# Optimization experiments

Hardware: AMD Instinct MI355X
Metric: run time of the kernel (lower is better)

Reference implementation:

```python
import jax, jax.numpy as jnp
import numpy as np

N_NODES = 100000
N_EDGES = 1600000
IN_DIM = 128
OUT_DIM = 128


def setup_inputs() -> dict:
    key = jax.random.key(0)
    k1, k2, k3, k4, k5 = jax.random.split(key, 5)
    h = jax.random.normal(k1, (N_NODES, IN_DIM), dtype=jnp.float32)
    # nn.Linear(in_dim, out_dim): W [out, in], b [out]
    W = jax.random.normal(k2, (OUT_DIM, IN_DIM), dtype=jnp.float32) * (1.0 / np.sqrt(IN_DIM))
    b = jax.random.normal(k3, (OUT_DIM,), dtype=jnp.float32) * 0.01
    edge_src = jax.random.randint(k4, (N_EDGES,), 0, N_NODES, dtype=jnp.int32)
    edge_dst = jax.random.randint(k5, (N_EDGES,), 0, N_NODES, dtype=jnp.int32)
    return {"h": h, "W": W, "b": b, "edge_src": edge_src, "edge_dst": edge_dst}


def reference(h, W, b, edge_src, edge_dst):
    n = h.shape[0]
    # in-degree of each node (edges point src -> dst), clamped to >= 1
    deg = jax.ops.segment_sum(jnp.ones_like(edge_dst, dtype=h.dtype), edge_dst, num_segments=n)
    norm = jnp.power(jnp.clip(deg, 1.0), -0.5)[:, None]  # [N, 1]
    hn = h * norm
    # copy_u + sum: gather source features, scatter-add to destinations (SpMM)
    agg = jax.ops.segment_sum(hn[edge_src], edge_dst, num_segments=n)  # [N, in_dim]
    out = (agg * norm) @ W.T + b
    return out
```

## Files before the change

kernel.cpp:

```cpp
#include <hip/hip_runtime.h>
#include <hip/hip_fp16.h>

#define DIM 128
#define TSH 8
#define TSZ 256
#define EBLK 4096

typedef _Float16 half8_t __attribute__((ext_vector_type(8)));
typedef float f32x4 __attribute__((ext_vector_type(4)));


__global__ __launch_bounds__(256) void hist_a(const int* __restrict__ dst,
                                              int* __restrict__ gh,
                                              int ne, int nblk, int nt) {
    __shared__ int h[512];
    int t = threadIdx.x;
    h[t] = 0; h[t + 256] = 0;
    __syncthreads();
    int i0 = blockIdx.x * EBLK + t;
#pragma unroll
    for (int u = 0; u < 16; ++u) {
        int i = i0 + u * 256;
        if (i < ne) atomicAdd(&h[dst[i] >> TSH], 1);
    }
    __syncthreads();
    for (int k = t; k < nt; k += 256) gh[k * nblk + blockIdx.x] = h[k];
}

__global__ __launch_bounds__(256) void scan_a(int* __restrict__ g,
                                              int* __restrict__ bsum, int M) {
    __shared__ int wsum[4];
    int t = threadIdx.x;
    int base = blockIdx.x * 1024 + t * 4;
    int4 v;
    if (base + 3 < M) v = *(const int4*)(g + base);
    else {
        v.x = (base + 0 < M) ? g[base + 0] : 0;
        v.y = (base + 1 < M) ? g[base + 1] : 0;
        v.z = (base + 2 < M) ? g[base + 2] : 0;
        v.w = (base + 3 < M) ? g[base + 3] : 0;
    }
    int s3 = v.x + v.y + v.z + v.w;
    int lane = t & 63, wv = t >> 6;
    int x = s3;
#pragma unroll
    for (int off = 1; off < 64; off <<= 1) {
        int y = __shfl_up(x, off, 64);
        if (lane >= off) x += y;
    }
    if (lane == 63) wsum[wv] = x;
    __syncthreads();
    int woff = 0;
    for (int i = 0; i < wv; ++i) woff += wsum[i];
    int ex = woff + x - s3;
    int4 o;
    o.x = ex; o.y = ex + v.x; o.z = o.y + v.y; o.w = o.z + v.z;
    if (base + 3 < M) *(int4*)(g + base) = o;
    else {
        if (base + 0 < M) g[base + 0] = o.x;
        if (base + 1 < M) g[base + 1] = o.y;
        if (base + 2 < M) g[base + 2] = o.z;
        if (base + 3 < M) g[base + 3] = o.w;
    }
    if (t == 0) bsum[blockIdx.x] = wsum[0] + wsum[1] + wsum[2] + wsum[3];
}

__global__ __launch_bounds__(256) void scanb_wprep(int* __restrict__ bsum, int nb,
                                                   const float* __restrict__ W,
                                                   _Float16* __restrict__ Wf) {
    if (blockIdx.x == 0) {
        __shared__ int s[256];
        int t = threadIdx.x;
        int d = (t < nb) ? bsum[t] : 0;
        s[t] = d;
        __syncthreads();
        for (int off = 1; off < 256; off <<= 1) {
            int v = (t >= off) ? s[t - off] : 0;
            __syncthreads();
            s[t] += v;
            __syncthreads();
        }
        if (t < nb) bsum[t] = s[t] - d;
    } else {
        int idx = (blockIdx.x - 1) * 256 + threadIdx.x;
        int tile = idx >> 8;
        int kk = (idx >> 6) & 3;
        int lane = idx & 63;
        int nn = lane & 15, quad = lane >> 4;
        const float* wr = W + (tile * 16 + nn) * DIM + kk * 32 + quad * 8;
        _Float16* o = Wf + (size_t)idx * 8;
#pragma unroll
        for (int j = 0; j < 8; ++j) o[j] = (_Float16)wr[j];
    }
}

__global__ __launch_bounds__(256) void scatter_b(const int* __restrict__ src,
                                                 const int* __restrict__ dst,
                                                 const int* __restrict__ gh,
                                                 const int* __restrict__ gb,
                                                 unsigned* __restrict__ tbuf,
                                                 int ne, int nblk) {
    __shared__ int h[512];
    int t = threadIdx.x;
    h[t] = 0; h[t + 256] = 0;
    __syncthreads();
    int i0 = blockIdx.x * EBLK + t;
#pragma unroll
    for (int u = 0; u < 16; ++u) {
        int i = i0 + u * 256;
        if (i < ne) {
            int d = dst[i];
            int key = d >> TSH;
            int r = atomicAdd(&h[key], 1);
            int idx = key * nblk + blockIdx.x;
            int pos = gh[idx] + gb[idx >> 10] + r;
            tbuf[pos] = ((unsigned)src[i] << TSH) | (unsigned)(d & (TSZ - 1));
        }
    }
}

__global__ __launch_bounds__(256) void tile_sort(const unsigned* __restrict__ tbuf,
                                                 const int* __restrict__ gh,
                                                 const int* __restrict__ gb,
                                                 int* __restrict__ ebuf,
                                                 int* __restrict__ row_start,
                                                 int n, int ne, int nblk, int nt) {
    __shared__ int hist[TSZ];
    __shared__ int cur[TSZ];
    __shared__ int ps[TSZ];
    int t = threadIdx.x;
    int tile = blockIdx.x;
    int i0 = tile * nblk;
    int ts = gh[i0] + gb[i0 >> 10];
    int i1 = (tile + 1) * nblk;
    int te = (tile + 1 < nt) ? gh[i1] + gb[i1 >> 10] : ne;
    hist[t] = 0;
    __syncthreads();
    for (int i = ts + t; i < te; i += 256)
        atomicAdd(&hist[tbuf[i] & (TSZ - 1)], 1);
    __syncthreads();
    int d = hist[t];
    ps[t] = d;
    __syncthreads();
    for (int off = 1; off < 256; off <<= 1) {
        int v = (t >= off) ? ps[t - off] : 0;
        __syncthreads();
        ps[t] += v;
        __syncthreads();
    }
    int ex = ps[t] - d;
    cur[t] = ex;
    int node = tile * TSZ + t;
    if (node <= n) row_start[node] = ts + ex;
    __syncthreads();
    for (int i = ts + t; i < te; i += 256) {
        unsigned p = tbuf[i];
        int dl = (int)(p & (TSZ - 1));
        int r = atomicAdd(&cur[dl], 1);
        ebuf[ts + r] = (int)(p >> TSH);
    }
}

__global__ __launch_bounds__(256) void hn_pack(const float* __restrict__ h,
                                               const int* __restrict__ rs,
                                               float2* __restrict__ hn, int n32) {
    int i = blockIdx.x * 256 + threadIdx.x;
    if (i >= n32) return;
    int node = i >> 5;
    int d = rs[node + 1] - rs[node];
    float sc = rsqrtf((float)(d > 1 ? d : 1));
    float4 v = ((const float4*)h)[i];
    union { __half2 h2[2]; float2 f2; } u;
    u.h2[0] = __floats2half2_rn(v.x * sc, v.y * sc);
    u.h2[1] = __floats2half2_rn(v.z * sc, v.w * sc);
    hn[i] = u.f2;
}

__global__ __launch_bounds__(512) void gather_gemm(const float2* __restrict__ hn,
                                                   const int* __restrict__ ebuf,
                                                   const int* __restrict__ rs,
                                                   const _Float16* __restrict__ Wf,
                                                   const float* __restrict__ b,
                                                   float* __restrict__ out, int n) {
    __shared__ _Float16 xs[64 * 136];
    int tid = threadIdx.x;
    int g = tid >> 5, lane = tid & 31;

#pragma unroll
    for (int it = 0; it < 4; ++it) {
        int row = it * 16 + g;
        int node = blockIdx.x * 64 + row;
        union { __half2 h2[2]; float2 f2; } u;
        if (node < n) {
            int s0 = rs[node];
            int s1 = rs[node + 1];
            __half2 a0 = __floats2half2_rn(0.f, 0.f), a1 = a0;
            int i = s0;
            for (; i + 7 < s1; i += 8) {
                int e0 = ebuf[i], e1 = ebuf[i + 1], e2 = ebuf[i + 2], e3 = ebuf[i + 3];
                int e4 = ebuf[i + 4], e5 = ebuf[i + 5], e6 = ebuf[i + 6], e7 = ebuf[i + 7];
                float2 r0 = hn[(size_t)e0 * 32 + lane];
                float2 r1 = hn[(size_t)e1 * 32 + lane];
                float2 r2 = hn[(size_t)e2 * 32 + lane];
                float2 r3 = hn[(size_t)e3 * 32 + lane];
                float2 r4 = hn[(size_t)e4 * 32 + lane];
                float2 r5 = hn[(size_t)e5 * 32 + lane];
                float2 r6 = hn[(size_t)e6 * 32 + lane];
                float2 r7 = hn[(size_t)e7 * 32 + lane];
                const __half2* q0 = (const __half2*)&r0;
                const __half2* q1 = (const __half2*)&r1;
                const __half2* q2 = (const __half2*)&r2;
                const __half2* q3 = (const __half2*)&r3;
                const __half2* q4 = (const __half2*)&r4;
                const __half2* q5 = (const __half2*)&r5;
                const __half2* q6 = (const __half2*)&r6;
                const __half2* q7 = (const __half2*)&r7;
                a0 = __hadd2(a0, q0[0]); a1 = __hadd2(a1, q0[1]);
                a0 = __hadd2(a0, q1[0]); a1 = __hadd2(a1, q1[1]);
                a0 = __hadd2(a0, q2[0]); a1 = __hadd2(a1, q2[1]);
                a0 = __hadd2(a0, q3[0]); a1 = __hadd2(a1, q3[1]);
                a0 = __hadd2(a0, q4[0]); a1 = __hadd2(a1, q4[1]);
                a0 = __hadd2(a0, q5[0]); a1 = __hadd2(a1, q5[1]);
                a0 = __hadd2(a0, q6[0]); a1 = __hadd2(a1, q6[1]);
                a0 = __hadd2(a0, q7[0]); a1 = __hadd2(a1, q7[1]);
            }
            for (; i + 3 < s1; i += 4) {
                int e0 = ebuf[i], e1 = ebuf[i + 1], e2 = ebuf[i + 2], e3 = ebuf[i + 3];
                float2 r0 = hn[(size_t)e0 * 32 + lane];
                float2 r1 = hn[(size_t)e1 * 32 + lane];
                float2 r2 = hn[(size_t)e2 * 32 + lane];
                float2 r3 = hn[(size_t)e3 * 32 + lane];
                const __half2* q0 = (const __half2*)&r0;
                const __half2* q1 = (const __half2*)&r1;
                const __half2* q2 = (const __half2*)&r2;
                const __half2* q3 = (const __half2*)&r3;
                a0 = __hadd2(a0, q0[0]); a1 = __hadd2(a1, q0[1]);
                a0 = __hadd2(a0, q1[0]); a1 = __hadd2(a1, q1[1]);
                a0 = __hadd2(a0, q2[0]); a1 = __hadd2(a1, q2[1]);
                a0 = __hadd2(a0, q3[0]); a1 = __hadd2(a1, q3[1]);
            }
            for (; i < s1; ++i) {
                int e0 = ebuf[i];
                float2 r0 = hn[(size_t)e0 * 32 + lane];
                const __half2* q0 = (const __half2*)&r0;
                a0 = __hadd2(a0, q0[0]); a1 = __hadd2(a1, q0[1]);
            }
            int dn = s1 - s0;
            float nd = rsqrtf((float)(dn > 1 ? dn : 1));
            float2 f0 = __half22float2(a0), f1 = __half22float2(a1);
            u.h2[0] = __floats2half2_rn(f0.x * nd, f0.y * nd);
            u.h2[1] = __floats2half2_rn(f1.x * nd, f1.y * nd);
        } else {
            u.h2[0] = __floats2half2_rn(0.f, 0.f);
            u.h2[1] = u.h2[0];
        }
        *(float2*)(xs + row * 136 + lane * 4) = u.f2;
    }
    __syncthreads();

    int w = tid >> 6;
    int wl = tid & 63;
    int cn = wl & 15;
    int quad = wl >> 4;

    f32x4 acc[4] = {{0.f, 0.f, 0.f, 0.f}, {0.f, 0.f, 0.f, 0.f},
                    {0.f, 0.f, 0.f, 0.f}, {0.f, 0.f, 0.f, 0.f}};
#pragma unroll
    for (int kk = 0; kk < 4; ++kk) {
        half8_t bf = ((const half8_t*)Wf)[(w * 4 + kk) * 64 + wl];
#pragma unroll
        for (int rt = 0; rt < 4; ++rt) {
            half8_t af = *(const half8_t*)(xs + (rt * 16 + cn) * 136 + kk * 32 + quad * 8);
            acc[rt] = __builtin_amdgcn_mfma_f32_16x16x32_f16(af, bf, acc[rt], 0, 0, 0);
        }
    }
    float bj = b[w * 16 + cn];
    int node0 = blockIdx.x * 64;
#pragma unroll
    for (int rt = 0; rt < 4; ++rt) {
#pragma unroll
        for (int r = 0; r < 4; ++r) {
            int node = node0 + rt * 16 + quad * 4 + r;
            if (node < n)
                out[(size_t)node * DIM + w * 16 + cn] = acc[rt][r] + bj;
        }
    }
}

extern "C" void kernel_launch(void* const* d_in, const int* in_sizes, int n_in,
                              void* d_out, int out_size, void* d_ws, size_t ws_size,
                              hipStream_t stream) {
    const float* h = (const float*)d_in[0];
    const float* W = (const float*)d_in[1];
    const float* b = (const float*)d_in[2];
    const int* esrc = (const int*)d_in[3];
    const int* edst = (const int*)d_in[4];
    float* out = (float*)d_out;

    int n = in_sizes[0] / DIM;
    int ne = in_sizes[3];

    int nblk = (ne + EBLK - 1) / EBLK;
    int nt = (n + TSZ - 1) >> TSH;
    int M = nt * nblk;
    int nsc = (M + 1023) / 1024;

    float2* hn = (float2*)d_ws;
    _Float16* Wf = (_Float16*)(hn + (size_t)n * 32);
    int* row_start = (int*)(Wf + 16384);
    int* gh = row_start + (n + 1);
    int* gbsum = gh + M;
    unsigned* tbuf = (unsigned*)(gbsum + 256);
    int* ebuf = (int*)(tbuf + ne);

    hist_a<<<nblk, 256, 0, stream>>>(edst, gh, ne, nblk, nt);
    scan_a<<<nsc, 256, 0, stream>>>(gh, gbsum, M);
    scanb_wprep<<<9, 256, 0, stream>>>(gbsum, nsc, W, Wf);
    scatter_b<<<nblk, 256, 0, stream>>>(esrc, edst, gh, gbsum, tbuf, ne, nblk);
    tile_sort<<<nt, 256, 0, stream>>>(tbuf, gh, gbsum, ebuf, row_start, n, ne, nblk, nt);
    hn_pack<<<(n * 32 + 255) / 256, 256, 0, stream>>>(h, row_start, hn, n * 32);
    gather_gemm<<<(n + 63) / 64, 512, 0, stream>>>(hn, ebuf, row_start, Wf, b, out, n);
}
```

Baseline: 239.4 us.

## Widen gather loads to 16-byte rows, 128-node tiles, nontemporal loads/stores

The gather now has 16 lanes per node, each loading 8 halves (16 bytes) per neighbour row instead of 32 lanes loading 8 bytes. The edge loop is unrolled by 16, and fp16 vector adds replace the half2 adds. Each block now covers 128 nodes, which doubles the MFMA row tiles per block and shares the W fragment loads across more rows. Nontemporal hints are added to the h read in hn_pack and to the output store, to keep streaming data from polluting cache; the trade-off is more registers and LDS per block, which may lower occupancy.

```diff
diff --git a/kernel.cpp b/kernel.cpp
--- a/kernel.cpp
+++ b/kernel.cpp
@@ -161,6 +161,7 @@
     }
 }
 
+typedef float f32x4v __attribute__((ext_vector_type(4)));
 __global__ __launch_bounds__(256) void hn_pack(const float* __restrict__ h,
                                                const int* __restrict__ rs,
                                                float2* __restrict__ hn, int n32) {
@@ -169,7 +170,7 @@
     int node = i >> 5;
     int d = rs[node + 1] - rs[node];
     float sc = rsqrtf((float)(d > 1 ? d : 1));
-    float4 v = ((const float4*)h)[i];
+    f32x4v v = __builtin_nontemporal_load((const f32x4v*)h + i);
     union { __half2 h2[2]; float2 f2; } u;
     u.h2[0] = __floats2half2_rn(v.x * sc, v.y * sc);
     u.h2[1] = __floats2half2_rn(v.z * sc, v.w * sc);
@@ -182,80 +183,57 @@
                                                    const _Float16* __restrict__ Wf,
                                                    const float* __restrict__ b,
                                                    float* __restrict__ out, int n) {
-    __shared__ _Float16 xs[64 * 136];
+    __shared__ _Float16 xs[128 * 136];
     int tid = threadIdx.x;
-    int g = tid >> 5, lane = tid & 31;
+    int g = tid >> 4, lane = tid & 15;
+    const _Float16* hp = (const _Float16*)hn + (lane << 3);
+
+#define LD_ROW(e) (*(const half8_t*)(hp + ((size_t)(unsigned)(e) << 7)))
 
 #pragma unroll
     for (int it = 0; it < 4; ++it) {
-        int row = it * 16 + g;
-        int node = blockIdx.x * 64 + row;
-        union { __half2 h2[2]; float2 f2; } u;
+        int row = it * 32 + g;
+        int node = blockIdx.x * 128 + row;
+        half8_t acc = {(_Float16)0, (_Float16)0, (_Float16)0, (_Float16)0,
+                       (_Float16)0, (_Float16)0, (_Float16)0, (_Float16)0};
         if (node < n) {
             int s0 = rs[node];
             int s1 = rs[node + 1];
-            __half2 a0 = __floats2half2_rn(0.f, 0.f), a1 = a0;
             int i = s0;
-            for (; i + 7 < s1; i += 8) {
-                int e0 = ebuf[i], e1 = ebuf[i + 1], e2 = ebuf[i + 2], e3 = ebuf[i + 3];
-                int e4 = ebuf[i + 4], e5 = ebuf[i + 5], e6 = ebuf[i + 6], e7 = ebuf[i + 7];
-                float2 r0 = hn[(size_t)e0 * 32 + lane];
-                float2 r1 = hn[(size_t)e1 * 32 + lane];
-                float2 r2 = hn[(size_t)e2 * 32 + lane];
-                float2 r3 = hn[(size_t)e3 * 32 + lane];
-                float2 r4 = hn[(size_t)e4 * 32 + lane];
-                float2 r5 = hn[(size_t)e5 * 32 + lane];
-                float2 r6 = hn[(size_t)e6 * 32 + lane];
-                float2 r7 = hn[(size_t)e7 * 32 + lane];
-                const __half2* q0 = (const __half2*)&r0;
-                const __half2* q1 = (const __half2*)&r1;
-                const __half2* q2 = (const __half2*)&r2;
-                const __half2* q3 = (const __half2*)&r3;
-                const __half2* q4 = (const __half2*)&r4;
-                const __half2* q5 = (const __half2*)&r5;
-                const __half2* q6 = (const __half2*)&r6;
-                const __half2* q7 = (const __half2*)&r7;
-                a0 = __hadd2(a0, q0[0]); a1 = __hadd2(a1, q0[1]);
-                a0 = __hadd2(a0, q1[0]); a1 = __hadd2(a1, q1[1]);
-                a0 = __hadd2(a0, q2[0]); a1 = __hadd2(a1, q2[1]);
-                a0 = __hadd2(a0, q3[0]); a1 = __hadd2(a1, q3[1]);
-                a0 = __hadd2(a0, q4[0]); a1 = __hadd2(a1, q4[1]);
-                a0 = __hadd2(a0, q5[0]); a1 = __hadd2(a1, q5[1]);
-                a0 = __hadd2(a0, q6[0]); a1 = __hadd2(a1, q6[1]);
-                a0 = __hadd2(a0, q7[0]); a1 = __hadd2(a1, q7[1]);
+            for (; i + 15 < s1; i += 16) {
+                int e0 = ebuf[i +  0], e1 = ebuf[i +  1], e2 = ebuf[i +  2], e3 = ebuf[i +  3];
+                int e4 = ebuf[i +  4], e5 = ebuf[i +  5], e6 = ebuf[i +  6], e7 = ebuf[i +  7];
+                int e8 = ebuf[i +  8], e9 = ebuf[i +  9], ea = ebuf[i + 10], eb = ebuf[i + 11];
+                int ec = ebuf[i + 12], ed = ebuf[i + 13], ee = ebuf[i + 14], ef = ebuf[i + 15];
+                half8_t r0 = LD_ROW(e0), r1 = LD_ROW(e1), r2 = LD_ROW(e2), r3 = LD_ROW(e3);
+                half8_t r4 = LD_ROW(e4), r5 = LD_ROW(e5), r6 = LD_ROW(e6), r7 = LD_ROW(e7);
+                half8_t r8 = LD_ROW(e8), r9 = LD_ROW(e9), ra = LD_ROW(ea), rb = LD_ROW(eb);
+                half8_t rc = LD_ROW(ec), rd = LD_ROW(ed), re = LD_ROW(ee), rf = LD_ROW(ef);
+                acc += r0; acc += r1; acc += r2; acc += r3;
+                acc += r4; acc += r5; acc += r6; acc += r7;
+                acc += r8; acc += r9; acc += ra; acc += rb;
+                acc += rc; acc += rd; acc += re; acc += rf;
             }
             for (; i + 3 < s1; i += 4) {
                 int e0 = ebuf[i], e1 = ebuf[i + 1], e2 = ebuf[i + 2], e3 = ebuf[i + 3];
-                float2 r0 = hn[(size_t)e0 * 32 + lane];
-                float2 r1 = hn[(size_t)e1 * 32 + lane];
-                float2 r2 = hn[(size_t)e2 * 32 + lane];
-                float2 r3 = hn[(size_t)e3 * 32 + lane];
-                const __half2* q0 = (const __half2*)&r0;
-                const __half2* q1 = (const __half2*)&r1;
-                const __half2* q2 = (const __half2*)&r2;
-                const __half2* q3 = (const __half2*)&r3;
-                a0 = __hadd2(a0, q0[0]); a1 = __hadd2(a1, q0[1]);
-                a0 = __hadd2(a0, q1[0]); a1 = __hadd2(a1, q1[1]);
-                a0 = __hadd2(a0, q2[0]); a1 = __hadd2(a1, q2[1]);
-                a0 = __hadd2(a0, q3[0]); a1 = __hadd2(a1, q3[1]);
+                half8_t r0 = LD_ROW(e0), r1 = LD_ROW(e1), r2 = LD_ROW(e2), r3 = LD_ROW(e3);
+                acc += r0; acc += r1; acc += r2; acc += r3;
             }
             for (; i < s1; ++i) {
-                int e0 = ebuf[i];
-                float2 r0 = hn[(size_t)e0 * 32 + lane];
-                const __half2* q0 = (const __half2*)&r0;
-                a0 = __hadd2(a0, q0[0]); a1 = __hadd2(a1, q0[1]);
+                half8_t r0 = LD_ROW(ebuf[i]);
+                acc += r0;
             }
             int dn = s1 - s0;
             float nd = rsqrtf((float)(dn > 1 ? dn : 1));
-            float2 f0 = __half22float2(a0), f1 = __half22float2(a1);
-            u.h2[0] = __floats2half2_rn(f0.x * nd, f0.y * nd);
-            u.h2[1] = __floats2half2_rn(f1.x * nd, f1.y * nd);
+            half8_t o;
+#pragma unroll
+            for (int j = 0; j < 8; ++j) o[j] = (_Float16)((float)acc[j] * nd);
+            *(half8_t*)(xs + row * 136 + lane * 8) = o;
         } else {
-            u.h2[0] = __floats2half2_rn(0.f, 0.f);
-            u.h2[1] = u.h2[0];
-        }
-        *(float2*)(xs + row * 136 + lane * 4) = u.f2;
-    }
+            *(half8_t*)(xs + row * 136 + lane * 8) = acc;
+        }
+    }
+#undef LD_ROW
     __syncthreads();
 
     int w = tid >> 6;
@@ -263,26 +241,29 @@
     int cn = wl & 15;
     int quad = wl >> 4;
 
-    f32x4 acc[4] = {{0.f, 0.f, 0.f, 0.f}, {0.f, 0.f, 0.f, 0.f},
+    f32x4 acc[8] = {{0.f, 0.f, 0.f, 0.f}, {0.f, 0.f, 0.f, 0.f},
+                    {0.f, 0.f, 0.f, 0.f}, {0.f, 0.f, 0.f, 0.f},
+                    {0.f, 0.f, 0.f, 0.f}, {0.f, 0.f, 0.f, 0.f},
                     {0.f, 0.f, 0.f, 0.f}, {0.f, 0.f, 0.f, 0.f}};
 #pragma unroll
     for (int kk = 0; kk < 4; ++kk) {
         half8_t bf = ((const half8_t*)Wf)[(w * 4 + kk) * 64 + wl];
 #pragma unroll
-        for (int rt = 0; rt < 4; ++rt) {
+        for (int rt = 0; rt < 8; ++rt) {
             half8_t af = *(const half8_t*)(xs + (rt * 16 + cn) * 136 + kk * 32 + quad * 8);
             acc[rt] = __builtin_amdgcn_mfma_f32_16x16x32_f16(af, bf, acc[rt], 0, 0, 0);
         }
     }
     float bj = b[w * 16 + cn];
-    int node0 = blockIdx.x * 64;
-#pragma unroll
-    for (int rt = 0; rt < 4; ++rt) {
+    int node0 = blockIdx.x * 128;
+#pragma unroll
+    for (int rt = 0; rt < 8; ++rt) {
 #pragma unroll
         for (int r = 0; r < 4; ++r) {
             int node = node0 + rt * 16 + quad * 4 + r;
             if (node < n)
-                out[(size_t)node * DIM + w * 16 + cn] = acc[rt][r] + bj;
+                __builtin_nontemporal_store(acc[rt][r] + bj,
+                                            &out[(size_t)node * DIM + w * 16 + cn]);
         }
     }
 }
@@ -319,5 +300,5 @@
     scatter_b<<<nblk, 256, 0, stream>>>(esrc, edst, gh, gbsum, tbuf, ne, nblk);
     tile_sort<<<nt, 256, 0, stream>>>(tbuf, gh, gbsum, ebuf, row_start, n, ne, nblk, nt);
     hn_pack<<<(n * 32 + 255) / 256, 256, 0, stream>>>(h, row_start, hn, n * 32);
-    gather_gemm<<<(n + 63) / 64, 512, 0, stream>>>(hn, ebuf, row_start, Wf, b, out, n);
-}
+    gather_gemm<<<(n + 127) / 128, 512, 0, stream>>>(hn, ebuf, row_start, Wf, b, out, n);
+}
```

Result: no change. 239.8 us (+0.2%).

## Stage scatter in LDS for coalesced tbuf writes; add nontemporal loads/stores

Applied to the files above, without the earlier changes.

scatter_b now computes each tile's per-block counts from the global prefix sums, runs a block-local scan, and sorts its edges by tile key into shared memory. It then writes them to tbuf in contiguous runs instead of scattering individual words. hn_pack reads h with nontemporal loads and gather_gemm writes out with nontemporal stores, to keep streaming data out of the cache. The cost is a larger shared-memory footprint in scatter_b, which can lower occupancy, plus an extra in-block scan with several barriers.

```diff
diff --git a/kernel.cpp b/kernel.cpp
--- a/kernel.cpp
+++ b/kernel.cpp
@@ -8,6 +8,7 @@
 
 typedef _Float16 half8_t __attribute__((ext_vector_type(8)));
 typedef float f32x4 __attribute__((ext_vector_type(4)));
+typedef float f32x4v __attribute__((ext_vector_type(4)));
 
 
 __global__ __launch_bounds__(256) void hist_a(const int* __restrict__ dst,
@@ -99,24 +100,72 @@
                                                  const int* __restrict__ gh,
                                                  const int* __restrict__ gb,
                                                  unsigned* __restrict__ tbuf,
-                                                 int ne, int nblk) {
+                                                 int ne, int nblk, int M, int nt) {
     __shared__ int h[512];
+    __shared__ int ps[512];
+    __shared__ int cur[512];
+    __shared__ unsigned sval[EBLK];
+    __shared__ unsigned short skey[EBLK];
     int t = threadIdx.x;
-    h[t] = 0; h[t + 256] = 0;
-    __syncthreads();
-    int i0 = blockIdx.x * EBLK + t;
+    int blk = blockIdx.x;
+
+    int p0a[2];
+#pragma unroll
+    for (int u = 0; u < 2; ++u) {
+        int k = t + u * 256;
+        int c = 0, p0 = 0;
+        if (k < nt) {
+            int idx = k * nblk + blk;
+            p0 = gh[idx] + gb[idx >> 10];
+            int p1 = (idx + 1 < M) ? (gh[idx + 1] + gb[(idx + 1) >> 10]) : ne;
+            c = p1 - p0;
+        }
+        h[k] = c;
+        p0a[u] = p0;
+    }
+    __syncthreads();
+    int h0 = h[2 * t];
+    int s2 = h0 + h[2 * t + 1];
+    ps[t] = s2;
+    __syncthreads();
+    for (int off = 1; off < 256; off <<= 1) {
+        int v = (t >= off) ? ps[t - off] : 0;
+        __syncthreads();
+        ps[t] += v;
+        __syncthreads();
+    }
+    int inc = ps[t];
+    __syncthreads();
+    int ex0 = inc - s2;
+    ps[2 * t] = ex0;
+    ps[2 * t + 1] = ex0 + h0;
+    cur[2 * t] = ex0;
+    cur[2 * t + 1] = ex0 + h0;
+    __syncthreads();
+#pragma unroll
+    for (int u = 0; u < 2; ++u) {
+        int k = t + u * 256;
+        h[k] = p0a[u] - ps[k];
+    }
+    __syncthreads();
+
+    int i0 = blk * EBLK + t;
 #pragma unroll
     for (int u = 0; u < 16; ++u) {
         int i = i0 + u * 256;
         if (i < ne) {
             int d = dst[i];
             int key = d >> TSH;
-            int r = atomicAdd(&h[key], 1);
-            int idx = key * nblk + blockIdx.x;
-            int pos = gh[idx] + gb[idx >> 10] + r;
-            tbuf[pos] = ((unsigned)src[i] << TSH) | (unsigned)(d & (TSZ - 1));
-        }
-    }
+            int r = atomicAdd(&cur[key], 1);
+            sval[r] = ((unsigned)src[i] << TSH) | (unsigned)(d & (TSZ - 1));
+            skey[r] = (unsigned short)key;
+        }
+    }
+    __syncthreads();
+    int cnt = ne - blk * EBLK;
+    if (cnt > EBLK) cnt = EBLK;
+    for (int p = t; p < cnt; p += 256)
+        tbuf[h[skey[p]] + p] = sval[p];
 }
 
 __global__ __launch_bounds__(256) void tile_sort(const unsigned* __restrict__ tbuf,
@@ -169,7 +218,7 @@
     int node = i >> 5;
     int d = rs[node + 1] - rs[node];
     float sc = rsqrtf((float)(d > 1 ? d : 1));
-    float4 v = ((const float4*)h)[i];
+    f32x4v v = __builtin_nontemporal_load((const f32x4v*)h + i);
     union { __half2 h2[2]; float2 f2; } u;
     u.h2[0] = __floats2half2_rn(v.x * sc, v.y * sc);
     u.h2[1] = __floats2half2_rn(v.z * sc, v.w * sc);
@@ -282,7 +331,8 @@
         for (int r = 0; r < 4; ++r) {
             int node = node0 + rt * 16 + quad * 4 + r;
             if (node < n)
-                out[(size_t)node * DIM + w * 16 + cn] = acc[rt][r] + bj;
+                __builtin_nontemporal_store(acc[rt][r] + bj,
+                                            &out[(size_t)node * DIM + w * 16 + cn]);
         }
     }
 }
@@ -316,7 +366,7 @@
     hist_a<<<nblk, 256, 0, stream>>>(edst, gh, ne, nblk, nt);
     scan_a<<<nsc, 256, 0, stream>>>(gh, gbsum, M);
     scanb_wprep<<<9, 256, 0, stream>>>(gbsum, nsc, W, Wf);
-    scatter_b<<<nblk, 256, 0, stream>>>(esrc, edst, gh, gbsum, tbuf, ne, nblk);
+    scatter_b<<<nblk, 256, 0, stream>>>(esrc, edst, gh, gbsum, tbuf, ne, nblk, M, nt);
     tile_sort<<<nt, 256, 0, stream>>>(tbuf, gh, gbsum, ebuf, row_start, n, ne, nblk, nt);
     hn_pack<<<(n * 32 + 255) / 256, 256, 0, stream>>>(h, row_start, hn, n * 32);
     gather_gemm<<<(n + 63) / 64, 512, 0, stream>>>(hn, ebuf, row_start, Wf, b, out, n);
```

Result: faster. 228.1 us (-4.7%).

## Replace two-level tiled counting sort with global-atomic CSR build

Applied to the files above, without the earlier changes.

Replaces the tiled histogram/scatter/tile-sort CSR construction with a per-node degree count using global atomics, a node-level prefix scan, and a scatter that claims slots with global atomic counters. The hn packing is fused into the scatter launch, and nontemporal loads and stores are used for h, ebuf and out. This cuts kernel launches and the intermediate tbuf pass, but relies on contended global atomics over 100k counters and makes the edge order within each row nondeterministic.

```diff
diff --git a/kernel.cpp b/kernel.cpp
--- a/kernel.cpp
+++ b/kernel.cpp
@@ -2,36 +2,44 @@
 #include <hip/hip_fp16.h>
 
 #define DIM 128
-#define TSH 8
-#define TSZ 256
-#define EBLK 4096
 
 typedef _Float16 half8_t __attribute__((ext_vector_type(8)));
 typedef float f32x4 __attribute__((ext_vector_type(4)));
-
-
-__global__ __launch_bounds__(256) void hist_a(const int* __restrict__ dst,
-                                              int* __restrict__ gh,
-                                              int ne, int nblk, int nt) {
-    __shared__ int h[512];
-    int t = threadIdx.x;
-    h[t] = 0; h[t + 256] = 0;
-    __syncthreads();
-    int i0 = blockIdx.x * EBLK + t;
-#pragma unroll
-    for (int u = 0; u < 16; ++u) {
-        int i = i0 + u * 256;
-        if (i < ne) atomicAdd(&h[dst[i] >> TSH], 1);
-    }
-    __syncthreads();
-    for (int k = t; k < nt; k += 256) gh[k * nblk + blockIdx.x] = h[k];
-}
-
-__global__ __launch_bounds__(256) void scan_a(int* __restrict__ g,
-                                              int* __restrict__ bsum, int M) {
-    __shared__ int wsum[4];
-    int t = threadIdx.x;
-    int base = blockIdx.x * 1024 + t * 4;
+typedef float f32x4v __attribute__((ext_vector_type(4)));
+
+#define EB1 2048
+#define EB3 2048
+
+
+__global__ __launch_bounds__(256) void k1_deg(const int* __restrict__ dst,
+                                              int* __restrict__ rs,
+                                              int ne,
+                                              const float* __restrict__ W,
+                                              _Float16* __restrict__ Wf) {
+    int blk = blockIdx.x;
+    int t = threadIdx.x;
+    if (blk >= EB1) {
+        int idx = (blk - EB1) * 256 + t;
+        int tile = idx >> 8;
+        int kk = (idx >> 6) & 3;
+        int lane = idx & 63;
+        int nn = lane & 15, quad = lane >> 4;
+        const float* wr = W + (tile * 16 + nn) * DIM + kk * 32 + quad * 8;
+        _Float16* o = Wf + (size_t)idx * 8;
+#pragma unroll
+        for (int j = 0; j < 8; ++j) o[j] = (_Float16)wr[j];
+        return;
+    }
+    int stride = EB1 * 256;
+    for (int i = blk * 256 + t; i < ne; i += stride)
+        atomicAdd(&rs[dst[i]], 1);
+}
+
+__global__ __launch_bounds__(512) void k2_scan(int* __restrict__ g,
+                                               int* __restrict__ bsum, int M) {
+    __shared__ int wsum[8];
+    int t = threadIdx.x;
+    int base = blockIdx.x * 2048 + t * 4;
     int4 v;
     if (base + 3 < M) v = *(const int4*)(g + base);
     else {
@@ -62,118 +70,70 @@
         if (base + 2 < M) g[base + 2] = o.z;
         if (base + 3 < M) g[base + 3] = o.w;
     }
-    if (t == 0) bsum[blockIdx.x] = wsum[0] + wsum[1] + wsum[2] + wsum[3];
-}
-
-__global__ __launch_bounds__(256) void scanb_wprep(int* __restrict__ bsum, int nb,
-                                                   const float* __restrict__ W,
-                                                   _Float16* __restrict__ Wf) {
-    if (blockIdx.x == 0) {
-        __shared__ int s[256];
-        int t = threadIdx.x;
-        int d = (t < nb) ? bsum[t] : 0;
-        s[t] = d;
-        __syncthreads();
-        for (int off = 1; off < 256; off <<= 1) {
-            int v = (t >= off) ? s[t - off] : 0;
-            __syncthreads();
-            s[t] += v;
-            __syncthreads();
-        }
-        if (t < nb) bsum[t] = s[t] - d;
-    } else {
-        int idx = (blockIdx.x - 1) * 256 + threadIdx.x;
-        int tile = idx >> 8;
-        int kk = (idx >> 6) & 3;
-        int lane = idx & 63;
-        int nn = lane & 15, quad = lane >> 4;
-        const float* wr = W + (tile * 16 + nn) * DIM + kk * 32 + quad * 8;
-        _Float16* o = Wf + (size_t)idx * 8;
-#pragma unroll
-        for (int j = 0; j < 8; ++j) o[j] = (_Float16)wr[j];
-    }
-}
-
-__global__ __launch_bounds__(256) void scatter_b(const int* __restrict__ src,
-                                                 const int* __restrict__ dst,
-                                                 const int* __restrict__ gh,
-                                                 const int* __restrict__ gb,
-                                                 unsigned* __restrict__ tbuf,
-                                                 int ne, int nblk) {
-    __shared__ int h[512];
-    int t = threadIdx.x;
-    h[t] = 0; h[t + 256] = 0;
+    if (t == 0) {
+        int s = 0;
+#pragma unroll
+        for (int i = 0; i < 8; ++i) s += wsum[i];
+        bsum[blockIdx.x] = s;
+    }
+}
+
+__global__ __launch_bounds__(256) void k3a_fix(int* __restrict__ rs,
+                                               int* __restrict__ cur,
+                                               const int* __restrict__ bsum,
+                                               int n, int nsc) {
+    __shared__ int gbl[64];
+    int t = threadIdx.x;
+    if (t < 64) {
+        int v = (t < nsc) ? bsum[t] : 0;
+        int x = v;
+#pragma unroll
+        for (int off = 1; off < 64; off <<= 1) {
+            int y = __shfl_up(x, off, 64);
+            if ((t & 63) >= off) x += y;
+        }
+        gbl[t] = x - v;
+    }
     __syncthreads();
-    int i0 = blockIdx.x * EBLK + t;
-#pragma unroll
-    for (int u = 0; u < 16; ++u) {
-        int i = i0 + u * 256;
-        if (i < ne) {
+    int i = blockIdx.x * 256 + t;
+    if (i <= n) {
+        int a = rs[i] + gbl[i >> 11];
+        rs[i] = a;
+        if (i < n) cur[i] = a;
+    }
+}
+
+__global__ __launch_bounds__(256) void k3b_scat(const int* __restrict__ src,
+                                                const int* __restrict__ dst,
+                                                int* __restrict__ cur,
+                                                int* __restrict__ ebuf,
+                                                const int* __restrict__ rs,
+                                                const float* __restrict__ h,
+                                                float2* __restrict__ hn,
+                                                int ne, int n32) {
+    int blk = blockIdx.x;
+    int t = threadIdx.x;
+    if (blk < EB3) {
+        int stride = EB3 * 256;
+        for (int i = blk * 256 + t; i < ne; i += stride) {
+            int s = src[i];
             int d = dst[i];
-            int key = d >> TSH;
-            int r = atomicAdd(&h[key], 1);
-            int idx = key * nblk + blockIdx.x;
-            int pos = gh[idx] + gb[idx >> 10] + r;
-            tbuf[pos] = ((unsigned)src[i] << TSH) | (unsigned)(d & (TSZ - 1));
-        }
-    }
-}
-
-__global__ __launch_bounds__(256) void tile_sort(const unsigned* __restrict__ tbuf,
-                                                 const int* __restrict__ gh,
-                                                 const int* __restrict__ gb,
-                                                 int* __restrict__ ebuf,
-                                                 int* __restrict__ row_start,
-                                                 int n, int ne, int nblk, int nt) {
-    __shared__ int hist[TSZ];
-    __shared__ int cur[TSZ];
-    __shared__ int ps[TSZ];
-    int t = threadIdx.x;
-    int tile = blockIdx.x;
-    int i0 = tile * nblk;
-    int ts = gh[i0] + gb[i0 >> 10];
-    int i1 = (tile + 1) * nblk;
-    int te = (tile + 1 < nt) ? gh[i1] + gb[i1 >> 10] : ne;
-    hist[t] = 0;
-    __syncthreads();
-    for (int i = ts + t; i < te; i += 256)
-        atomicAdd(&hist[tbuf[i] & (TSZ - 1)], 1);
-    __syncthreads();
-    int d = hist[t];
-    ps[t] = d;
-    __syncthreads();
-    for (int off = 1; off < 256; off <<= 1) {
-        int v = (t >= off) ? ps[t - off] : 0;
-        __syncthreads();
-        ps[t] += v;
-        __syncthreads();
-    }
-    int ex = ps[t] - d;
-    cur[t] = ex;
-    int node = tile * TSZ + t;
-    if (node <= n) row_start[node] = ts + ex;
-    __syncthreads();
-    for (int i = ts + t; i < te; i += 256) {
-        unsigned p = tbuf[i];
-        int dl = (int)(p & (TSZ - 1));
-        int r = atomicAdd(&cur[dl], 1);
-        ebuf[ts + r] = (int)(p >> TSH);
-    }
-}
-
-__global__ __launch_bounds__(256) void hn_pack(const float* __restrict__ h,
-                                               const int* __restrict__ rs,
-                                               float2* __restrict__ hn, int n32) {
-    int i = blockIdx.x * 256 + threadIdx.x;
-    if (i >= n32) return;
-    int node = i >> 5;
-    int d = rs[node + 1] - rs[node];
-    float sc = rsqrtf((float)(d > 1 ? d : 1));
-    float4 v = ((const float4*)h)[i];
-    union { __half2 h2[2]; float2 f2; } u;
-    u.h2[0] = __floats2half2_rn(v.x * sc, v.y * sc);
-    u.h2[1] = __floats2half2_rn(v.z * sc, v.w * sc);
-    hn[i] = u.f2;
+            int pos = atomicAdd(&cur[d], 1);
+            __builtin_nontemporal_store(s, &ebuf[pos]);
+        }
+        return;
+    }
+    int i = (blk - EB3) * 256 + t;
+    if (i < n32) {
+        int node = i >> 5;
+        int dg = rs[node + 1] - rs[node];
+        float sc = rsqrtf((float)(dg > 1 ? dg : 1));
+        f32x4v v = __builtin_nontemporal_load((const f32x4v*)h + i);
+        union { __half2 h2[2]; float2 f2; } u;
+        u.h2[0] = __floats2half2_rn(v.x * sc, v.y * sc);
+        u.h2[1] = __floats2half2_rn(v.z * sc, v.w * sc);
+        hn[i] = u.f2;
+    }
 }
 
 __global__ __launch_bounds__(512) void gather_gemm(const float2* __restrict__ hn,
@@ -282,7 +242,8 @@
         for (int r = 0; r < 4; ++r) {
             int node = node0 + rt * 16 + quad * 4 + r;
             if (node < n)
-                out[(size_t)node * DIM + w * 16 + cn] = acc[rt][r] + bj;
+                __builtin_nontemporal_store(acc[rt][r] + bj,
+                                            &out[(size_t)node * DIM + w * 16 + cn]);
         }
     }
 }
@@ -299,25 +260,23 @@
 
     int n = in_sizes[0] / DIM;
     int ne = in_sizes[3];
-
-    int nblk = (ne + EBLK - 1) / EBLK;
-    int nt = (n + TSZ - 1) >> TSH;
-    int M = nt * nblk;
-    int nsc = (M + 1023) / 1024;
+    int n32 = n * 32;
 
     float2* hn = (float2*)d_ws;
     _Float16* Wf = (_Float16*)(hn + (size_t)n * 32);
     int* row_start = (int*)(Wf + 16384);
-    int* gh = row_start + (n + 1);
-    int* gbsum = gh + M;
-    unsigned* tbuf = (unsigned*)(gbsum + 256);
-    int* ebuf = (int*)(tbuf + ne);
-
-    hist_a<<<nblk, 256, 0, stream>>>(edst, gh, ne, nblk, nt);
-    scan_a<<<nsc, 256, 0, stream>>>(gh, gbsum, M);
-    scanb_wprep<<<9, 256, 0, stream>>>(gbsum, nsc, W, Wf);
-    scatter_b<<<nblk, 256, 0, stream>>>(esrc, edst, gh, gbsum, tbuf, ne, nblk);
-    tile_sort<<<nt, 256, 0, stream>>>(tbuf, gh, gbsum, ebuf, row_start, n, ne, nblk, nt);
-    hn_pack<<<(n * 32 + 255) / 256, 256, 0, stream>>>(h, row_start, hn, n * 32);
+    int* cur = row_start + ((n + 4) & ~3);
+    int* bsum = cur + ((n + 3) & ~3);
+    int* ebuf = bsum + 64;
+
+    int M = n + 1;
+    int nsc = (M + 2047) / 2048;
+
+    hipMemsetAsync(row_start, 0, (size_t)(n + 1) * sizeof(int), stream);
+    k1_deg<<<EB1 + 8, 256, 0, stream>>>(edst, row_start, ne, W, Wf);
+    k2_scan<<<nsc, 512, 0, stream>>>(row_start, bsum, M);
+    k3a_fix<<<(M + 255) / 256, 256, 0, stream>>>(row_start, cur, bsum, n, nsc);
+    k3b_scat<<<EB3 + (n32 + 255) / 256, 256, 0, stream>>>(esrc, edst, cur, ebuf,
+                                                          row_start, h, hn, ne, n32);
     gather_gemm<<<(n + 63) / 64, 512, 0, stream>>>(hn, ebuf, row_start, Wf, b, out, n);
 }
```

Measured after the change: 414.5 us. +73.1%, slower.
